# Optimization experiments

Hardware: AMD Instinct MI355X
Metric: run time of the kernel (lower is better)

Reference implementation:

```python
import jax, jax.numpy as jnp
import numpy as np

N = 8192          # num nodes
F = 256           # feature_size
D = 128           # graph_embedding_size
E = 262144        # num edges (avg degree 32)
SLOPE = 0.2       # cfg.negativeslope
NEG_INF = -9e15   # matches torch's -9000000000000000.0 mask value


def setup_inputs() -> dict:
    key = jax.random.key(0)
    k1, k2, k3, k4 = jax.random.split(key, 4)
    X = jax.random.normal(k1, (N, F), dtype=jnp.float32)
    edge_index = jax.random.randint(k2, (2, E), 0, N, dtype=jnp.int64)
    # glorot init for Ws, xavier_uniform(gain=1.414) for a
    lim_ws = np.sqrt(6.0 / (F + D)).astype(np.float32)
    Ws = jax.random.uniform(k3, (F, D), jnp.float32, -lim_ws, lim_ws)
    lim_a = (1.414 * np.sqrt(6.0 / (2 * D + 1))).astype(np.float32)
    a = jax.random.uniform(k4, (2 * D, 1), jnp.float32, -lim_a, lim_a)
    return {"edge_index": edge_index, "X": X, "Ws": Ws, "a": a}


def reference(edge_index, X, Ws, a):
    # dense adjacency mask from edge list (sparse_coo_tensor(...).to_dense())
    adj = jnp.zeros((N, N), jnp.float32).at[edge_index[0], edge_index[1]].set(1.0)
    Wh = X @ Ws                                   # [N, D]
    # GAT-style score: Wh1_i + Wh2_j, then leaky relu
    e = jax.nn.leaky_relu(Wh @ a[:D] + (Wh @ a[D:]).T, SLOPE)  # [N, N]
    scores = jnp.where(adj > 0, e, NEG_INF)
    att = jax.nn.softmax(scores, axis=1)          # masked row softmax
    return jax.nn.elu(att @ Wh)                   # [N, D]
```

## Files before the change

kernel.cpp:

```cpp
#include <hip/hip_runtime.h>
#include <math.h>

#define N_NODES 8192
#define FDIM 256
#define DDIM 128
#define SLOPE 0.2f
#define WPR 256
#define MAXD 128

typedef __attribute__((ext_vector_type(8))) short bf16x8;
typedef __attribute__((ext_vector_type(4))) float f32x4;

__device__ __forceinline__ unsigned short f2bf(float f) {
    unsigned u = __float_as_uint(f);
    u += 0x7fffu + ((u >> 16) & 1u);
    return (unsigned short)(u >> 16);
}
__device__ __forceinline__ float bf2f(unsigned short h) {
    return __uint_as_float(((unsigned)h) << 16);
}

__global__ __launch_bounds__(256) void prep_k(const float* __restrict__ Ws,
                                              unsigned short* __restrict__ Bphi,
                                              unsigned short* __restrict__ Bplo,
                                              unsigned* __restrict__ bm) {
    int b = blockIdx.x, t = threadIdx.x;
    size_t zi = (size_t)b * 256 + t;
    uint4 z = make_uint4(0u, 0u, 0u, 0u);
#pragma unroll
    for (int k = 0; k < 8; k++) ((uint4*)bm)[(size_t)k * 65536 + zi] = z;

    if (b >= 16) return;
    int tid = b * 256 + t;
    int ct = tid >> 9, ks = (tid >> 6) & 7, l = tid & 63;
    int kbase = ks * 32 + (l >> 4) * 8;
    int col = ct * 16 + (l & 15);
    bf16x8 h, lo;
#pragma unroll
    for (int e = 0; e < 8; e++) {
        float v = Ws[(size_t)(kbase + e) * DDIM + col];
        unsigned short hq = f2bf(v);
        h[e] = (short)hq;
        lo[e] = (short)f2bf(v - bf2f(hq));
    }
    *(bf16x8*)(Bphi + (size_t)tid * 8) = h;
    *(bf16x8*)(Bplo + (size_t)tid * 8) = lo;
}

__global__ __launch_bounds__(256) void mega_k(const int* __restrict__ edge, int E,
                                              const float* __restrict__ X,
                                              const unsigned short* __restrict__ Bphi,
                                              const unsigned short* __restrict__ Bplo,
                                              const float* __restrict__ a,
                                              unsigned short* __restrict__ WhB,
                                              float* __restrict__ s1,
                                              float* __restrict__ s2,
                                              unsigned* __restrict__ bm) {
    __shared__ unsigned short Ah[16 * 264], Al[16 * 264];
    __shared__ float ps1[64], ps2[64];
    int bid = blockIdx.x, t = threadIdx.x;

    if (bid >= 512) {
        int e = (bid - 512) * 256 + t;
        if (e < E) {
            int r = edge[e];
            int c = edge[E + e];
            atomicOr(&bm[(size_t)r * WPR + (c >> 5)], 1u << (c & 31));
        }
        return;
    }

    int w = t >> 6, lane = t & 63, lr = lane & 15, kg = lane >> 4;
    int row0 = bid * 16;

    const float4* Xg = (const float4*)(X + (size_t)row0 * FDIM);
#pragma unroll
    for (int i = 0; i < 4; i++) {
        int lin = t + 256 * i;
        int r = lin >> 6, q = lin & 63;
        float4 v = Xg[r * 64 + q];
        ushort4 h, l;
        h.x = f2bf(v.x); l.x = f2bf(v.x - bf2f(h.x));
        h.y = f2bf(v.y); l.y = f2bf(v.y - bf2f(h.y));
        h.z = f2bf(v.z); l.z = f2bf(v.z - bf2f(h.z));
        h.w = f2bf(v.w); l.w = f2bf(v.w - bf2f(h.w));
        *(ushort4*)(Ah + r * 264 + q * 4) = h;
        *(ushort4*)(Al + r * 264 + q * 4) = l;
    }
    __syncthreads();

    f32x4 acc0 = (f32x4){0.f, 0.f, 0.f, 0.f};
    f32x4 acc1 = (f32x4){0.f, 0.f, 0.f, 0.f};
    int ct0 = 2 * w, ct1 = 2 * w + 1;

#pragma unroll 2
    for (int ks = 0; ks < 8; ks++) {
        bf16x8 ahi = *(bf16x8*)(Ah + lr * 264 + ks * 32 + kg * 8);
        bf16x8 alo = *(bf16x8*)(Al + lr * 264 + ks * 32 + kg * 8);
        size_t o0 = (size_t)((ct0 * 8 + ks) * 64 + lane) * 8;
        size_t o1 = (size_t)((ct1 * 8 + ks) * 64 + lane) * 8;
        bf16x8 bh0 = *(const bf16x8*)(Bphi + o0);
        bf16x8 bl0 = *(const bf16x8*)(Bplo + o0);
        bf16x8 bh1 = *(const bf16x8*)(Bphi + o1);
        bf16x8 bl1 = *(const bf16x8*)(Bplo + o1);
        acc0 = __builtin_amdgcn_mfma_f32_16x16x32_bf16(ahi, bh0, acc0, 0, 0, 0);
        acc0 = __builtin_amdgcn_mfma_f32_16x16x32_bf16(ahi, bl0, acc0, 0, 0, 0);
        acc0 = __builtin_amdgcn_mfma_f32_16x16x32_bf16(alo, bh0, acc0, 0, 0, 0);
        acc1 = __builtin_amdgcn_mfma_f32_16x16x32_bf16(ahi, bh1, acc1, 0, 0, 0);
        acc1 = __builtin_amdgcn_mfma_f32_16x16x32_bf16(ahi, bl1, acc1, 0, 0, 0);
        acc1 = __builtin_amdgcn_mfma_f32_16x16x32_bf16(alo, bh1, acc1, 0, 0, 0);
    }

#pragma unroll
    for (int r = 0; r < 4; r++) {
        int row = row0 + kg * 4 + r;
        int c0 = ct0 * 16 + lr, c1 = ct1 * 16 + lr;
        float v0 = acc0[r], v1 = acc1[r];
        WhB[(size_t)row * DDIM + c0] = f2bf(v0);
        WhB[(size_t)row * DDIM + c1] = f2bf(v1);
        float q1 = v0 * a[c0] + v1 * a[c1];
        float q2 = v0 * a[DDIM + c0] + v1 * a[DDIM + c1];
        for (int o = 1; o < 16; o <<= 1) {
            q1 += __shfl_xor(q1, o, 16);
            q2 += __shfl_xor(q2, o, 16);
        }
        if (lr == 0) { ps1[w * 16 + kg * 4 + r] = q1; ps2[w * 16 + kg * 4 + r] = q2; }
    }
    __syncthreads();
    if (t < 16) {
        s1[row0 + t] = (ps1[t] + ps1[16 + t]) + (ps1[32 + t] + ps1[48 + t]);
        s2[row0 + t] = (ps2[t] + ps2[16 + t]) + (ps2[32 + t] + ps2[48 + t]);
    }
}

__global__ __launch_bounds__(256) void row_bm_k(const unsigned* __restrict__ bm,
                                                const float* __restrict__ s1v,
                                                const float* __restrict__ s2v,
                                                const unsigned short* __restrict__ WhB,
                                                float* __restrict__ out) {
    __shared__ float    pe[4][MAXD];
    __shared__ unsigned jl[4][MAXD];
    __shared__ unsigned lcnt[4];

    int w = threadIdx.x >> 6, lane = threadIdx.x & 63;
    int i = blockIdx.x * 4 + w;
    const ushort2* WhB2 = (const ushort2*)WhB;

    if (lane == 0) lcnt[w] = 0u;
    float s1i = s1v[i];
    uint4 wd = ((const uint4*)(bm + (size_t)i * WPR))[lane];

    float lmax = -3e38f;
#pragma unroll
    for (int q = 0; q < 4; q++) {
        unsigned x = (&wd.x)[q];
        int base = (lane * 4 + q) * 32;
        while (x) {
            int bpos = __ffs(x) - 1; x &= x - 1;
            unsigned j = (unsigned)(base + bpos);
            float e = s1i + s2v[j];
            e = e > 0.f ? e : SLOPE * e;
            lmax = fmaxf(lmax, e);
            unsigned pos = atomicAdd(&lcnt[w], 1u);
            if (pos < MAXD) { jl[w][pos] = j; pe[w][pos] = e; }
        }
    }
    for (int o = 32; o; o >>= 1) lmax = fmaxf(lmax, __shfl_xor(lmax, o, 64));
    unsigned deg = lcnt[w];
    if (deg > MAXD) deg = MAXD;

    if (deg == 0u) {
        float sx = 0.f, sy = 0.f;
        for (int rr = 0; rr < N_NODES; rr++) {
            ushort2 u = WhB2[(size_t)rr * 64 + lane];
            sx += bf2f(u.x); sy += bf2f(u.y);
        }
        sx *= (1.0f / N_NODES); sy *= (1.0f / N_NODES);
        sx = sx > 0.f ? sx : __expf(sx) - 1.f;
        sy = sy > 0.f ? sy : __expf(sy) - 1.f;
        ((float2*)out)[(size_t)i * 64 + lane] = make_float2(sx, sy);
        return;
    }

    float lsum = 0.f;
    for (unsigned n = lane; n < deg; n += 64) {
        float p = __expf(pe[w][n] - lmax);
        pe[w][n] = p;
        lsum += p;
    }
    for (int o = 32; o; o >>= 1) lsum += __shfl_xor(lsum, o, 64);
    float inv = 1.0f / lsum;

    float ax = 0.f, ay = 0.f;
#pragma unroll 8
    for (unsigned n = 0; n < deg; ++n) {
        float p = pe[w][n];
        unsigned j = jl[w][n];
        ushort2 u = WhB2[(size_t)j * 64 + lane];
        ax = fmaf(p, bf2f(u.x), ax);
        ay = fmaf(p, bf2f(u.y), ay);
    }
    ax *= inv; ay *= inv;
    ax = ax > 0.f ? ax : __expf(ax) - 1.f;
    ay = ay > 0.f ? ay : __expf(ay) - 1.f;
    ((float2*)out)[(size_t)i * 64 + lane] = make_float2(ax, ay);
}

extern "C" void kernel_launch(void* const* d_in, const int* in_sizes, int n_in,
                              void* d_out, int out_size, void* d_ws, size_t ws_size,
                              hipStream_t stream) {
    const int*   edge = (const int*)d_in[0];
    const float* X    = (const float*)d_in[1];
    const float* Ws   = (const float*)d_in[2];
    const float* a    = (const float*)d_in[3];
    float*       out  = (float*)d_out;
    int E = in_sizes[0] / 2;

    char* ws = (char*)d_ws;
    size_t off = 0;
    unsigned*       bm   = (unsigned*)(ws + off); off += (size_t)N_NODES * WPR * 4;
    float*          s1   = (float*)(ws + off);    off += N_NODES * 4;
    float*          s2   = (float*)(ws + off);    off += N_NODES * 4;
    unsigned short* WhB  = (unsigned short*)(ws + off); off += (size_t)N_NODES * DDIM * 2;
    unsigned short* Bphi = (unsigned short*)(ws + off); off += (size_t)FDIM * DDIM * 2;
    unsigned short* Bplo = (unsigned short*)(ws + off); off += (size_t)FDIM * DDIM * 2;

    int nbuild = (E + 255) / 256;
    prep_k<<<256, 256, 0, stream>>>(Ws, Bphi, Bplo, bm);
    mega_k<<<512 + nbuild, 256, 0, stream>>>(edge, E, X, Bphi, Bplo, a, WhB, s1, s2, bm);
    row_bm_k<<<N_NODES / 4, 256, 0, stream>>>(bm, s1, s2, WhB, out);
}
```

Baseline: 40.51 us.

## Replace dense adjacency bitmap with per-XCD replicated ELL edge lists

The 8 MB dense row bitmap, which had to be zeroed and then scanned in full, is replaced by per-row neighbor lists with counters, replicated eight ways by the XCC id of the writing workgroup to spread atomic contention. The row kernel gathers up to 32 entries from each replica, deduplicates them with a per-wave LDS bitmap, and then runs the same softmax and aggregation as before. This removes the large memset and the bitmap scan. In exchange, any row with more than 32 edges landing in one replica silently drops the excess neighbors, and the per-edge atomicAdd returns a value, which can be slower than a fire-and-forget atomicOr.

```diff
diff --git a/kernel.cpp b/kernel.cpp
--- a/kernel.cpp
+++ b/kernel.cpp
@@ -5,8 +5,9 @@
 #define FDIM 256
 #define DDIM 128
 #define SLOPE 0.2f
-#define WPR 256
 #define MAXD 128
+#define RSL 32
+#define NREP 8
 
 typedef __attribute__((ext_vector_type(8))) short bf16x8;
 typedef __attribute__((ext_vector_type(4))) float f32x4;
@@ -23,12 +24,10 @@
 __global__ __launch_bounds__(256) void prep_k(const float* __restrict__ Ws,
                                               unsigned short* __restrict__ Bphi,
                                               unsigned short* __restrict__ Bplo,
-                                              unsigned* __restrict__ bm) {
+                                              unsigned* __restrict__ cnt8) {
     int b = blockIdx.x, t = threadIdx.x;
-    size_t zi = (size_t)b * 256 + t;
-    uint4 z = make_uint4(0u, 0u, 0u, 0u);
-#pragma unroll
-    for (int k = 0; k < 8; k++) ((uint4*)bm)[(size_t)k * 65536 + zi] = z;
+    int zi = b * 256 + t;
+    if (zi < NREP * N_NODES / 4) ((uint4*)cnt8)[zi] = make_uint4(0u, 0u, 0u, 0u);
 
     if (b >= 16) return;
     int tid = b * 256 + t;
@@ -37,11 +36,11 @@
     int col = ct * 16 + (l & 15);
     bf16x8 h, lo;
 #pragma unroll
-    for (int e = 0; e < 8; e++) {
-        float v = Ws[(size_t)(kbase + e) * DDIM + col];
+    for (int q = 0; q < 8; q++) {
+        float v = Ws[(size_t)(kbase + q) * DDIM + col];
         unsigned short hq = f2bf(v);
-        h[e] = (short)hq;
-        lo[e] = (short)f2bf(v - bf2f(hq));
+        h[q] = (short)hq;
+        lo[q] = (short)f2bf(v - bf2f(hq));
     }
     *(bf16x8*)(Bphi + (size_t)tid * 8) = h;
     *(bf16x8*)(Bplo + (size_t)tid * 8) = lo;
@@ -55,17 +54,23 @@
                                               unsigned short* __restrict__ WhB,
                                               float* __restrict__ s1,
                                               float* __restrict__ s2,
-                                              unsigned* __restrict__ bm) {
+                                              unsigned* __restrict__ cnt8,
+                                              unsigned* __restrict__ ell8) {
     __shared__ unsigned short Ah[16 * 264], Al[16 * 264];
     __shared__ float ps1[64], ps2[64];
     int bid = blockIdx.x, t = threadIdx.x;
 
     if (bid >= 512) {
+        unsigned xcd;
+        asm volatile("s_getreg_b32 %0, hwreg(HW_REG_XCC_ID)" : "=s"(xcd));
+        xcd &= 7u;
         int e = (bid - 512) * 256 + t;
         if (e < E) {
             int r = edge[e];
             int c = edge[E + e];
-            atomicOr(&bm[(size_t)r * WPR + (c >> 5)], 1u << (c & 31));
+            size_t rowk = (size_t)xcd * N_NODES + (unsigned)r;
+            unsigned slot = atomicAdd(&cnt8[rowk], 1u);
+            if (slot < RSL) ell8[rowk * RSL + slot] = (unsigned)c;
         }
         return;
     }
@@ -133,11 +138,13 @@
     }
 }
 
-__global__ __launch_bounds__(256) void row_bm_k(const unsigned* __restrict__ bm,
-                                                const float* __restrict__ s1v,
-                                                const float* __restrict__ s2v,
-                                                const unsigned short* __restrict__ WhB,
-                                                float* __restrict__ out) {
+__global__ __launch_bounds__(256) void row_wave_k(const unsigned* __restrict__ cnt8,
+                                                  const unsigned* __restrict__ ell8,
+                                                  const float* __restrict__ s1v,
+                                                  const float* __restrict__ s2v,
+                                                  const unsigned short* __restrict__ WhB,
+                                                  float* __restrict__ out) {
+    __shared__ unsigned bmw[4][256];
     __shared__ float    pe[4][MAXD];
     __shared__ unsigned jl[4][MAXD];
     __shared__ unsigned lcnt[4];
@@ -146,23 +153,27 @@
     int i = blockIdx.x * 4 + w;
     const ushort2* WhB2 = (const ushort2*)WhB;
 
+    ((uint4*)bmw[w])[lane] = make_uint4(0u, 0u, 0u, 0u);
     if (lane == 0) lcnt[w] = 0u;
     float s1i = s1v[i];
-    uint4 wd = ((const uint4*)(bm + (size_t)i * WPR))[lane];
-
     float lmax = -3e38f;
-#pragma unroll
-    for (int q = 0; q < 4; q++) {
-        unsigned x = (&wd.x)[q];
-        int base = (lane * 4 + q) * 32;
-        while (x) {
-            int bpos = __ffs(x) - 1; x &= x - 1;
-            unsigned j = (unsigned)(base + bpos);
-            float e = s1i + s2v[j];
-            e = e > 0.f ? e : SLOPE * e;
-            lmax = fmaxf(lmax, e);
-            unsigned pos = atomicAdd(&lcnt[w], 1u);
-            if (pos < MAXD) { jl[w][pos] = j; pe[w][pos] = e; }
+
+#pragma unroll
+    for (int k = 0; k < NREP; k++) {
+        size_t rowk = (size_t)k * N_NODES + i;
+        unsigned dk = cnt8[rowk];
+        if (dk > RSL) dk = RSL;
+        if (lane < (int)dk) {
+            unsigned j = ell8[rowk * RSL + lane];
+            unsigned m = 1u << (j & 31);
+            unsigned old = atomicOr(&bmw[w][j >> 5], m);
+            if (!(old & m)) {
+                float e = s1i + s2v[j];
+                e = e > 0.f ? e : SLOPE * e;
+                lmax = fmaxf(lmax, e);
+                unsigned pos = atomicAdd(&lcnt[w], 1u);
+                if (pos < MAXD) { jl[w][pos] = j; pe[w][pos] = e; }
+            }
         }
     }
     for (int o = 32; o; o >>= 1) lmax = fmaxf(lmax, __shfl_xor(lmax, o, 64));
@@ -218,7 +229,8 @@
 
     char* ws = (char*)d_ws;
     size_t off = 0;
-    unsigned*       bm   = (unsigned*)(ws + off); off += (size_t)N_NODES * WPR * 4;
+    unsigned*       cnt8 = (unsigned*)(ws + off); off += (size_t)NREP * N_NODES * 4;
+    unsigned*       ell8 = (unsigned*)(ws + off); off += (size_t)NREP * N_NODES * RSL * 4;
     float*          s1   = (float*)(ws + off);    off += N_NODES * 4;
     float*          s2   = (float*)(ws + off);    off += N_NODES * 4;
     unsigned short* WhB  = (unsigned short*)(ws + off); off += (size_t)N_NODES * DDIM * 2;
@@ -226,7 +238,7 @@
     unsigned short* Bplo = (unsigned short*)(ws + off); off += (size_t)FDIM * DDIM * 2;
 
     int nbuild = (E + 255) / 256;
-    prep_k<<<256, 256, 0, stream>>>(Ws, Bphi, Bplo, bm);
-    mega_k<<<512 + nbuild, 256, 0, stream>>>(edge, E, X, Bphi, Bplo, a, WhB, s1, s2, bm);
-    row_bm_k<<<N_NODES / 4, 256, 0, stream>>>(bm, s1, s2, WhB, out);
-}
+    prep_k<<<256, 256, 0, stream>>>(Ws, Bphi, Bplo, cnt8);
+    mega_k<<<512 + nbuild, 256, 0, stream>>>(edge, E, X, Bphi, Bplo, a, WhB, s1, s2, cnt8, ell8);
+    row_wave_k<<<N_NODES / 4, 256, 0, stream>>>(cnt8, ell8, s1, s2, WhB, out);
+}
```

New measurement: 44.53 us. +9.9%, slower.
